# Performance work log

Measured on AMD Instinct MI355X. Metric: run time of the kernel, lower is better.

Reference implementation:

```python
import jax, jax.numpy as jnp
import numpy as np

Q_OFFSET = 128  # stored quants are in [0,255); subtract to get signed int8 range


def setup_inputs() -> dict:
    key = jax.random.key(0)
    k1, k2, k3, k4 = jax.random.split(key, 4)
    O, NB, BS = 4096, 128, 32  # out_features, num_blocks, block_size (Q8_0)
    x = jax.random.normal(k1, (4, 1024, NB * BS), dtype=jnp.float16)
    q_weight = jax.random.randint(k2, (O, NB, BS), 0, 255, dtype=jnp.int32)
    scales = jax.random.uniform(k3, (O, NB), dtype=jnp.float16) * jnp.float16(0.05)
    bias = jax.random.normal(k4, (O,), dtype=jnp.float16)
    return {"x": x, "q_weight": q_weight, "scales": scales, "bias": bias}


def reference(x, q_weight, scales, bias):
    # GGUF Q8_0-style on-the-fly dequant: w[o, b*32+j] = (q[o,b,j]-128) * scale[o,b]
    q = q_weight.astype(jnp.float16) - jnp.float16(Q_OFFSET)  # [O, NB, BS]
    w = (q * scales[:, :, None]).reshape(scales.shape[0], -1)  # [O, I]
    # linear: y = x @ w^T + bias
    return jnp.einsum('bsi,oi->bso', x, w) + bias
```

## Files before the change

kernel.cpp:

```cpp
#include <hip/hip_runtime.h>
#include <stdint.h>


#define QOFF 128

typedef __bf16 bf16_t;
typedef __bf16 bf16x8 __attribute__((ext_vector_type(8)));
typedef float f32x4 __attribute__((ext_vector_type(4)));

#define W_LGKM0 0xC07F
#define W_VM4 0x0F74
#define W_VM0 0x0F70

__global__ __launch_bounds__(256) void prep_kernel(
    const int* __restrict__ q, const float* __restrict__ scales,
    const float* __restrict__ X, bf16_t* __restrict__ W,
    bf16_t* __restrict__ Xb, int K, int NB, int nDeq) {
  const int b = blockIdx.x;
  if (b < nDeq) {
    const size_t e = ((size_t)b * 256 + threadIdx.x) * 8;
    const int o = (int)(e / (size_t)K);
    const int i = (int)(e % (size_t)K);
    const float s = scales[o * NB + (i >> 5)];
    int4 a = *(const int4*)(q + e);
    int4 c = *(const int4*)(q + e + 4);
    const int* av = (const int*)&a;
    const int* cv = (const int*)&c;
    bf16x8 t;
#pragma unroll
    for (int j = 0; j < 4; ++j) t[j] = (bf16_t)((float)(av[j] - QOFF) * s);
#pragma unroll
    for (int j = 0; j < 4; ++j) t[4 + j] = (bf16_t)((float)(cv[j] - QOFF) * s);
    *(bf16x8*)(W + e) = t;
  } else {
    const size_t e = ((size_t)(b - nDeq) * 256 + threadIdx.x) * 8;
    float4 a = *(const float4*)(X + e);
    float4 c = *(const float4*)(X + e + 4);
    bf16x8 t;
    t[0] = (bf16_t)a.x; t[1] = (bf16_t)a.y; t[2] = (bf16_t)a.z; t[3] = (bf16_t)a.w;
    t[4] = (bf16_t)c.x; t[5] = (bf16_t)c.y; t[6] = (bf16_t)c.z; t[7] = (bf16_t)c.w;
    *(bf16x8*)(Xb + e) = t;
  }
}

__device__ __forceinline__ void async16(bf16_t* lds, const bf16_t* g) {
  __builtin_amdgcn_global_load_lds(
      (const __attribute__((address_space(1))) unsigned int*)(const void*)g,
      (__attribute__((address_space(3))) unsigned int*)(void*)lds, 16, 0, 0);
}

template <int QM, int QN>
__device__ __forceinline__ void mm_block(f32x4 (&acc)[8][4],
                                         const bf16x8 (&af)[4][2],
                                         const bf16x8 (&bv)[2][2]) {
  __builtin_amdgcn_s_setprio(1);
#pragma unroll
  for (int ks = 0; ks < 2; ++ks)
#pragma unroll
    for (int fi = 0; fi < 4; ++fi)
#pragma unroll
      for (int fj = 0; fj < 2; ++fj)
        acc[QM * 4 + fi][QN * 2 + fj] = __builtin_amdgcn_mfma_f32_16x16x32_bf16(
            af[fi][ks], bv[fj][ks], acc[QM * 4 + fi][QN * 2 + fj], 0, 0, 0);
  __builtin_amdgcn_s_setprio(0);
}

__device__ __forceinline__ void rd_a(const bf16_t* base, const int* swz,
                                     bf16x8 (&af)[4][2]) {
#pragma unroll
  for (int fi = 0; fi < 4; ++fi)
#pragma unroll
    for (int ks = 0; ks < 2; ++ks)
      af[fi][ks] = *(const bf16x8*)(base + fi * 1024 + swz[ks]);
}

__device__ __forceinline__ void rd_b(const bf16_t* base, const int* swz,
                                     bf16x8 (&bv)[2][2]) {
#pragma unroll
  for (int fj = 0; fj < 2; ++fj)
#pragma unroll
    for (int ks = 0; ks < 2; ++ks)
      bv[fj][ks] = *(const bf16x8*)(base + fj * 1024 + swz[ks]);
}

__global__ __launch_bounds__(512, 2) void gemm_8ph(
    const bf16_t* __restrict__ A,
    const bf16_t* __restrict__ B,
    const float* __restrict__ bias,
    float* __restrict__ C,
    int M, int N, int K) {
  __shared__ bf16_t lsA[2][256 * 64];
  __shared__ bf16_t lsB[2][256 * 64];

  const int tid = threadIdx.x;
  const int lane = tid & 63;
  const int wave = tid >> 6;
  const int r = lane & 15;
  const int qd = lane >> 4;
  const int wm = (wave >> 2) * 128;
  const int wn = (wave & 3) * 64;

  const int nbx = N >> 8;
  const int nwg = gridDim.x;
  int wg = blockIdx.x;
  if ((nwg & 7) == 0) wg = (wg & 7) * (nwg >> 3) + (wg >> 3);
  const int m0 = (wg / nbx) * 256;
  const int n0 = (wg % nbx) * 256;

  f32x4 acc[8][4] = {};

  const int srow = tid >> 3;
  const int sslot = (tid & 7) ^ (srow & 7);
  const bf16_t* gA0 = A + (size_t)(m0 + srow) * K + sslot * 8;
  const bf16_t* gB0 = B + (size_t)(n0 + srow) * K + sslot * 8;

  auto stgA = [&](bf16_t* dstTile, int half, int koff) {
    bf16_t* d = dstTile + half * 8192 + tid * 8;
    const bf16_t* g = gA0 + (size_t)(half * 128) * K + koff;
    async16(d, g);
    async16(d + 4096, g + 64 * (size_t)K);
  };
  auto stgB = [&](bf16_t* dstTile, int half, int koff) {
    bf16_t* d = dstTile + half * 8192 + tid * 8;
    const bf16_t* g = gB0 + (size_t)(half * 128) * K + koff;
    async16(d, g);
    async16(d + 4096, g + 64 * (size_t)K);
  };

  const int swz[2] = {(qd ^ (r & 7)) * 8, ((4 + qd) ^ (r & 7)) * 8};
  const bf16_t* a0base = &lsA[0][(wm + r) * 64];
  const bf16_t* a1base = &lsA[1][(wm + r) * 64];
  const bf16_t* b0base = &lsB[0][(wn + r) * 64];
  const bf16_t* b1base = &lsB[1][(wn + r) * 64];

  const int NT = K >> 6;
  const int NITER = NT >> 1;

  stgA(lsA[0], 0, 0);
  stgA(lsA[0], 1, 0);
  stgB(lsB[0], 0, 0);
  stgB(lsB[0], 1, 0);
  stgB(lsB[1], 0, 64);
  stgB(lsB[1], 1, 64);
  __builtin_amdgcn_s_waitcnt(W_VM4);
  __builtin_amdgcn_s_barrier();

  bf16x8 af[4][2], bf0[2][2], bf1[2][2];

#pragma unroll 1
  for (int j = 0; j < NITER; ++j) {
    const int k1 = (2 * j + 1) * 64;
    int t2 = 2 * j + 2; if (t2 >= NT) t2 -= NT;
    int t3 = 2 * j + 3; if (t3 >= NT) t3 -= NT;
    const int k2 = t2 * 64;
    const int k3 = t3 * 64;

    rd_a(a0base, swz, af);
    rd_b(b0base, swz, bf0);
    stgA(lsA[1], 0, k1);
    __builtin_amdgcn_s_barrier();
    __builtin_amdgcn_s_waitcnt(W_LGKM0);
    mm_block<0, 0>(acc, af, bf0);
    __builtin_amdgcn_s_barrier();
    rd_b(b0base + 2048, swz, bf1);
    stgA(lsA[1], 1, k1);
    __builtin_amdgcn_s_barrier();
    __builtin_amdgcn_s_waitcnt(W_LGKM0);
    mm_block<0, 1>(acc, af, bf1);
    __builtin_amdgcn_s_barrier();
    rd_a(a0base + 4096, swz, af);
    stgB(lsB[0], 0, k2);
    __builtin_amdgcn_s_barrier();
    __builtin_amdgcn_s_waitcnt(W_LGKM0);
    mm_block<1, 1>(acc, af, bf1);
    __builtin_amdgcn_s_barrier();
    stgB(lsB[0], 1, k2);
    __builtin_amdgcn_s_barrier();
    mm_block<1, 0>(acc, af, bf0);
    __builtin_amdgcn_s_waitcnt(W_VM4);
    __builtin_amdgcn_s_barrier();

    rd_a(a1base, swz, af);
    rd_b(b1base, swz, bf0);
    stgA(lsA[0], 0, k2);
    __builtin_amdgcn_s_barrier();
    __builtin_amdgcn_s_waitcnt(W_LGKM0);
    mm_block<0, 0>(acc, af, bf0);
    __builtin_amdgcn_s_barrier();
    rd_b(b1base + 2048, swz, bf1);
    stgA(lsA[0], 1, k2);
    __builtin_amdgcn_s_barrier();
    __builtin_amdgcn_s_waitcnt(W_LGKM0);
    mm_block<0, 1>(acc, af, bf1);
    __builtin_amdgcn_s_barrier();
    rd_a(a1base + 4096, swz, af);
    stgB(lsB[1], 0, k3);
    __builtin_amdgcn_s_barrier();
    __builtin_amdgcn_s_waitcnt(W_LGKM0);
    mm_block<1, 1>(acc, af, bf1);
    __builtin_amdgcn_s_barrier();
    stgB(lsB[1], 1, k3);
    __builtin_amdgcn_s_barrier();
    mm_block<1, 0>(acc, af, bf0);
    __builtin_amdgcn_s_waitcnt(W_VM4);
    __builtin_amdgcn_s_barrier();
  }

  __builtin_amdgcn_s_waitcnt(W_VM0);

#pragma unroll
  for (int ni = 0; ni < 4; ++ni) {
    const int n = n0 + wn + ni * 16 + r;
    const float bv = bias[n];
#pragma unroll
    for (int mi = 0; mi < 8; ++mi) {
      const int mbase = m0 + wm + mi * 16 + qd * 4;
#pragma unroll
      for (int reg = 0; reg < 4; ++reg) {
        C[(size_t)(mbase + reg) * N + n] = acc[mi][ni][reg] + bv;
      }
    }
  }
}

__global__ __launch_bounds__(256) void gemm_db(
    const bf16_t* __restrict__ A, const bf16_t* __restrict__ B,
    const float* __restrict__ bias, float* __restrict__ C, int M, int N,
    int K) {
  __shared__ bf16_t lsA[2][128 * 32];
  __shared__ bf16_t lsB[2][128 * 32];

  const int tid = threadIdx.x;
  const int lane = tid & 63;
  const int wave = tid >> 6;
  const int m0 = blockIdx.y * 128;
  const int n0 = blockIdx.x * 128;
  const int wm = (wave >> 1) * 64;
  const int wn = (wave & 1) * 64;
  const int r = lane & 15;
  const int qd = lane >> 4;

  f32x4 acc[4][4] = {};

  const int e0 = tid * 8;
  const int e1 = 2048 + tid * 8;
  const bf16_t* gA0 = A + (size_t)(m0 + (e0 >> 5)) * K + (e0 & 31);
  const bf16_t* gA1 = A + (size_t)(m0 + (e1 >> 5)) * K + (e1 & 31);
  const bf16_t* gB0 = B + (size_t)(n0 + (e0 >> 5)) * K + (e0 & 31);
  const bf16_t* gB1 = B + (size_t)(n0 + (e1 >> 5)) * K + (e1 & 31);

  async16(&lsA[0][e0], gA0);
  async16(&lsA[0][e1], gA1);
  async16(&lsB[0][e0], gB0);
  async16(&lsB[0][e1], gB1);

  int buf = 0;
  for (int k0 = 0; k0 < K; k0 += 32, buf ^= 1) {
    __syncthreads();
    if (k0 + 32 < K) {
      const int nk = k0 + 32;
      async16(&lsA[buf ^ 1][e0], gA0 + nk);
      async16(&lsA[buf ^ 1][e1], gA1 + nk);
      async16(&lsB[buf ^ 1][e0], gB0 + nk);
      async16(&lsB[buf ^ 1][e1], gB1 + nk);
    }
    bf16x8 af[4], bfv[4];
#pragma unroll
    for (int i = 0; i < 4; ++i) {
      af[i] = *(const bf16x8*)&lsA[buf][(wm + i * 16 + r) * 32 + qd * 8];
      bfv[i] = *(const bf16x8*)&lsB[buf][(wn + i * 16 + r) * 32 + qd * 8];
    }
#pragma unroll
    for (int mi = 0; mi < 4; ++mi)
#pragma unroll
      for (int ni = 0; ni < 4; ++ni)
        acc[mi][ni] = __builtin_amdgcn_mfma_f32_16x16x32_bf16(
            af[mi], bfv[ni], acc[mi][ni], 0, 0, 0);
  }

#pragma unroll
  for (int ni = 0; ni < 4; ++ni) {
    const int n = n0 + wn + ni * 16 + r;
    const float bv = bias[n];
#pragma unroll
    for (int mi = 0; mi < 4; ++mi) {
      const int mbase = m0 + wm + mi * 16 + qd * 4;
#pragma unroll
      for (int reg = 0; reg < 4; ++reg) {
        C[(size_t)(mbase + reg) * N + n] = acc[mi][ni][reg] + bv;
      }
    }
  }
}

__global__ __launch_bounds__(256) void gemm_fused(
    const float* __restrict__ Af, const int* __restrict__ q,
    const float* __restrict__ scales, const float* __restrict__ bias,
    float* __restrict__ C, int M, int N, int K, int NB) {
  __shared__ bf16_t lsA[128 * 32];
  __shared__ bf16_t lsB[128 * 32];

  const int tid = threadIdx.x;
  const int lane = tid & 63;
  const int wave = tid >> 6;
  const int m0 = blockIdx.y * 128;
  const int n0 = blockIdx.x * 128;
  const int wm = (wave >> 1) * 64;
  const int wn = (wave & 1) * 64;
  const int r = lane & 15;
  const int qd = lane >> 4;

  const int e = tid * 16;
  const int row = e >> 5;
  const int col = e & 31;

  const float* gAf = Af + (size_t)(m0 + row) * K + col;
  const int* gQ = q + (size_t)(n0 + row) * K + col;
  const float* gS = scales + (size_t)(n0 + row) * NB;

  f32x4 acc[4][4] = {};

  for (int k0 = 0; k0 < K; k0 += 32) {
    bf16x8 a0, a1, b0, b1;
    {
      float4 f0 = *(const float4*)(gAf + k0);
      float4 f1 = *(const float4*)(gAf + k0 + 4);
      float4 f2 = *(const float4*)(gAf + k0 + 8);
      float4 f3 = *(const float4*)(gAf + k0 + 12);
      a0[0] = (bf16_t)f0.x; a0[1] = (bf16_t)f0.y; a0[2] = (bf16_t)f0.z; a0[3] = (bf16_t)f0.w;
      a0[4] = (bf16_t)f1.x; a0[5] = (bf16_t)f1.y; a0[6] = (bf16_t)f1.z; a0[7] = (bf16_t)f1.w;
      a1[0] = (bf16_t)f2.x; a1[1] = (bf16_t)f2.y; a1[2] = (bf16_t)f2.z; a1[3] = (bf16_t)f2.w;
      a1[4] = (bf16_t)f3.x; a1[5] = (bf16_t)f3.y; a1[6] = (bf16_t)f3.z; a1[7] = (bf16_t)f3.w;
    }
    {
      const float s = gS[k0 >> 5];
      int qv[16];
      *(int4*)&qv[0] = *(const int4*)(gQ + k0);
      *(int4*)&qv[4] = *(const int4*)(gQ + k0 + 4);
      *(int4*)&qv[8] = *(const int4*)(gQ + k0 + 8);
      *(int4*)&qv[12] = *(const int4*)(gQ + k0 + 12);
#pragma unroll
      for (int j = 0; j < 8; ++j) b0[j] = (bf16_t)((float)(qv[j] - QOFF) * s);
#pragma unroll
      for (int j = 0; j < 8; ++j)
        b1[j] = (bf16_t)((float)(qv[8 + j] - QOFF) * s);
    }

    __syncthreads();
    *(bf16x8*)&lsA[e] = a0;
    *(bf16x8*)&lsA[e + 8] = a1;
    *(bf16x8*)&lsB[e] = b0;
    *(bf16x8*)&lsB[e + 8] = b1;
    __syncthreads();

    bf16x8 af[4], bfv[4];
#pragma unroll
    for (int i = 0; i < 4; ++i) {
      af[i] = *(const bf16x8*)&lsA[(wm + i * 16 + r) * 32 + qd * 8];
      bfv[i] = *(const bf16x8*)&lsB[(wn + i * 16 + r) * 32 + qd * 8];
    }
#pragma unroll
    for (int mi = 0; mi < 4; ++mi)
#pragma unroll
      for (int ni = 0; ni < 4; ++ni)
        acc[mi][ni] = __builtin_amdgcn_mfma_f32_16x16x32_bf16(
            af[mi], bfv[ni], acc[mi][ni], 0, 0, 0);
  }

#pragma unroll
  for (int ni = 0; ni < 4; ++ni) {
    const int n = n0 + wn + ni * 16 + r;
    const float bv = bias[n];
#pragma unroll
    for (int mi = 0; mi < 4; ++mi) {
      const int mbase = m0 + wm + mi * 16 + qd * 4;
#pragma unroll
      for (int reg = 0; reg < 4; ++reg) {
        C[(size_t)(mbase + reg) * N + n] = acc[mi][ni][reg] + bv;
      }
    }
  }
}

extern "C" void kernel_launch(void* const* d_in, const int* in_sizes, int n_in,
                              void* d_out, int out_size, void* d_ws,
                              size_t ws_size, hipStream_t stream) {
  const float* x = (const float*)d_in[0];
  const int* qw = (const int*)d_in[1];
  const float* scales = (const float*)d_in[2];
  const float* bias = (const float*)d_in[3];
  float* out = (float*)d_out;

  const int O = in_sizes[3];
  const int K = in_sizes[1] / O;
  const int NB = in_sizes[2] / O;
  const int M = in_sizes[0] / K;
  (void)n_in; (void)out_size;

  const size_t Wbytes = (size_t)O * K * sizeof(bf16_t);
  const size_t Xbytes = (size_t)M * K * sizeof(bf16_t);

  if (ws_size >= Wbytes + Xbytes) {
    bf16_t* W = (bf16_t*)d_ws;
    bf16_t* Xb = (bf16_t*)((char*)d_ws + Wbytes);
    const int nDeq = (int)((size_t)O * K / 2048);
    const int nCvt = (int)((size_t)M * K / 2048);
    prep_kernel<<<nDeq + nCvt, 256, 0, stream>>>(qw, scales, x, W, Xb, K, NB,
                                                 nDeq);
    if ((M % 256) == 0 && (O % 256) == 0 && (K % 128) == 0) {
      const int nwg = (M / 256) * (O / 256);
      gemm_8ph<<<nwg, 512, 0, stream>>>(Xb, W, bias, out, M, O, K);
    } else {
      dim3 grid(O / 128, M / 128);
      gemm_db<<<grid, 256, 0, stream>>>(Xb, W, bias, out, M, O, K);
    }
  } else {
    dim3 grid(O / 128, M / 128);
    gemm_fused<<<grid, 256, 0, stream>>>(x, qw, scales, bias, out, M, O, K,
                                         NB);
  }
}
```

Before: 298.5 us.

## Drop mid-phase barriers and explicit lgkm waits; interleave LDS fragment reads

Removes the barrier and the explicit lgkmcnt(0) wait placed before each MFMA block, so the compiler inserts finer-grained waits and waves are no longer forced to lockstep between LDS reads and math. The A and B LDS fragment reads are reordered and interleaved by k-slice so the first MFMAs can start while the later reads are still in flight. The risk is that staging writes into the other LDS buffer are now less strictly ordered against reads by other waves, and that the scheduler may put its waits in worse places.

```diff
diff --git a/kernel.cpp b/kernel.cpp
--- a/kernel.cpp
+++ b/kernel.cpp
@@ -8,7 +8,6 @@
 typedef __bf16 bf16x8 __attribute__((ext_vector_type(8)));
 typedef float f32x4 __attribute__((ext_vector_type(4)));
 
-#define W_LGKM0 0xC07F
 #define W_VM4 0x0F74
 #define W_VM0 0x0F70
 
@@ -68,19 +67,33 @@
 __device__ __forceinline__ void rd_a(const bf16_t* base, const int* swz,
                                      bf16x8 (&af)[4][2]) {
 #pragma unroll
-  for (int fi = 0; fi < 4; ++fi)
-#pragma unroll
-    for (int ks = 0; ks < 2; ++ks)
+  for (int ks = 0; ks < 2; ++ks)
+#pragma unroll
+    for (int fi = 0; fi < 4; ++fi)
       af[fi][ks] = *(const bf16x8*)(base + fi * 1024 + swz[ks]);
 }
 
 __device__ __forceinline__ void rd_b(const bf16_t* base, const int* swz,
                                      bf16x8 (&bv)[2][2]) {
 #pragma unroll
-  for (int fj = 0; fj < 2; ++fj)
-#pragma unroll
-    for (int ks = 0; ks < 2; ++ks)
+  for (int ks = 0; ks < 2; ++ks)
+#pragma unroll
+    for (int fj = 0; fj < 2; ++fj)
       bv[fj][ks] = *(const bf16x8*)(base + fj * 1024 + swz[ks]);
+}
+
+__device__ __forceinline__ void rd12(const bf16_t* abase, const bf16_t* bbase,
+                                     const int* swz, bf16x8 (&af)[4][2],
+                                     bf16x8 (&bv)[2][2]) {
+#pragma unroll
+  for (int ks = 0; ks < 2; ++ks) {
+    af[0][ks] = *(const bf16x8*)(abase + swz[ks]);
+    bv[0][ks] = *(const bf16x8*)(bbase + swz[ks]);
+    af[1][ks] = *(const bf16x8*)(abase + 1024 + swz[ks]);
+    bv[1][ks] = *(const bf16x8*)(bbase + 1024 + swz[ks]);
+    af[2][ks] = *(const bf16x8*)(abase + 2048 + swz[ks]);
+    af[3][ks] = *(const bf16x8*)(abase + 3072 + swz[ks]);
+  }
 }
 
 __global__ __launch_bounds__(512, 2) void gemm_8ph(
@@ -155,52 +168,36 @@
     const int k2 = t2 * 64;
     const int k3 = t3 * 64;
 
-    rd_a(a0base, swz, af);
-    rd_b(b0base, swz, bf0);
+    rd12(a0base, b0base, swz, af, bf0);
     stgA(lsA[1], 0, k1);
-    __builtin_amdgcn_s_barrier();
-    __builtin_amdgcn_s_waitcnt(W_LGKM0);
     mm_block<0, 0>(acc, af, bf0);
     __builtin_amdgcn_s_barrier();
     rd_b(b0base + 2048, swz, bf1);
     stgA(lsA[1], 1, k1);
-    __builtin_amdgcn_s_barrier();
-    __builtin_amdgcn_s_waitcnt(W_LGKM0);
     mm_block<0, 1>(acc, af, bf1);
     __builtin_amdgcn_s_barrier();
     rd_a(a0base + 4096, swz, af);
     stgB(lsB[0], 0, k2);
-    __builtin_amdgcn_s_barrier();
-    __builtin_amdgcn_s_waitcnt(W_LGKM0);
     mm_block<1, 1>(acc, af, bf1);
     __builtin_amdgcn_s_barrier();
     stgB(lsB[0], 1, k2);
-    __builtin_amdgcn_s_barrier();
     mm_block<1, 0>(acc, af, bf0);
     __builtin_amdgcn_s_waitcnt(W_VM4);
     __builtin_amdgcn_s_barrier();
 
-    rd_a(a1base, swz, af);
-    rd_b(b1base, swz, bf0);
+    rd12(a1base, b1base, swz, af, bf0);
     stgA(lsA[0], 0, k2);
-    __builtin_amdgcn_s_barrier();
-    __builtin_amdgcn_s_waitcnt(W_LGKM0);
     mm_block<0, 0>(acc, af, bf0);
     __builtin_amdgcn_s_barrier();
     rd_b(b1base + 2048, swz, bf1);
     stgA(lsA[0], 1, k2);
-    __builtin_amdgcn_s_barrier();
-    __builtin_amdgcn_s_waitcnt(W_LGKM0);
     mm_block<0, 1>(acc, af, bf1);
     __builtin_amdgcn_s_barrier();
     rd_a(a1base + 4096, swz, af);
     stgB(lsB[1], 0, k3);
-    __builtin_amdgcn_s_barrier();
-    __builtin_amdgcn_s_waitcnt(W_LGKM0);
     mm_block<1, 1>(acc, af, bf1);
     __builtin_amdgcn_s_barrier();
     stgB(lsB[1], 1, k3);
-    __builtin_amdgcn_s_barrier();
     mm_block<1, 0>(acc, af, bf0);
     __builtin_amdgcn_s_waitcnt(W_VM4);
     __builtin_amdgcn_s_barrier();
```

Result: faster. 292.5 us (-2.0%).
